# Performance work log

Hardware: AMD Instinct MI355X
Metric: run time of the kernel (lower is better)

The kernel has to match this reference:

```python
import jax, jax.numpy as jnp
import numpy as np
import math

MODEL_DIM = 2048
NUM_EXPERTS = 64
N_TOKENS = 16384
CAPACITY_FACTOR = 1.0
MIN_CAPACITY = 8
THRESHOLD = 0.5


def _threshold_gating(logits):
    # Faithful jax translation of main_thresholdGating (training path, threshold>0).
    # Note: the torch code truncates sorted columns to the data-dependent
    # explore_top_k_num; we keep the full E columns instead. This is exactly
    # equivalent: dropped columns are all-unchosen (importance 0), and using
    # arange(E,0,-1) instead of arange(K,0,-1) shifts every chosen importance
    # by the same constant (E-K), which preserves the per-expert top-k order.
    N, E = logits.shape
    capacity = max(int(math.ceil(N / E * CAPACITY_FACTOR)), MIN_CAPACITY)  # static

    gates = jax.nn.softmax(logits, axis=1)                    # [N,E]
    indices1 = jnp.argmax(gates, axis=1)                      # top-1 expert per token
    mask1 = jax.nn.one_hot(indices1, E, dtype=gates.dtype)    # [N,E]

    # sorted gates + cumsum threshold selection
    gates_sorted, gates_idx = jax.lax.top_k(gates, E)         # [N,E] descending
    cum = jnp.cumsum(gates_sorted, axis=-1)
    chosen = (cum - gates_sorted) < THRESHOLD                 # [N,E] bool
    chosen = chosen.at[:, 0].set(True)                        # always keep top-1

    # scatter importance = rank-priority + gate prob into expert columns
    rank_imp = jnp.arange(E, 0, -1, dtype=gates.dtype)[None, :] + gates_sorted
    imp = jnp.where(chosen, rank_imp, jnp.zeros_like(rank_imp))
    row = jnp.arange(N)[:, None]
    # gates_idx rows are permutations of experts -> no scatter collisions
    tam = jnp.zeros((N, E), gates.dtype).at[row, gates_idx].set(imp)  # [N,E]

    # capacity truncation: per expert column keep the `capacity` tokens with
    # highest importance
    top_idx = jax.lax.top_k(tam.T, capacity)[1]               # [E, capacity]
    keep = jnp.zeros((N, E), gates.dtype).at[top_idx, jnp.arange(E)[:, None]].set(1.0)
    final_mask = ((tam * keep) > 0).astype(gates.dtype)       # [N,E]

    combine_weights = gates * final_mask

    # load-balancing aux loss (GShard style)
    me = jnp.mean(gates, axis=0)
    ce = jnp.mean(mask1, axis=0)
    l_aux = jnp.sum(me * ce) * E
    return l_aux, combine_weights


def setup_inputs() -> dict:
    key = jax.random.key(0)
    kx, kw = jax.random.split(key)
    x = jax.random.normal(kx, (N_TOKENS, MODEL_DIM), dtype=jnp.float32)
    # gate weight of wg = Linear(model_dim, num_experts, bias=False)
    W = jax.random.normal(kw, (NUM_EXPERTS, MODEL_DIM), dtype=jnp.float32) / math.sqrt(MODEL_DIM)
    return {"x": x, "W": W}


def reference(x, W):
    logits = x @ W.T                                          # [N,E]
    l_aux, combine_weights = _threshold_gating(logits)
    return l_aux, combine_weights
```

## Files before the change

kernel.cpp:

```cpp
#include <hip/hip_runtime.h>
#include <cstdint>
#include <cstddef>

#define N_TOK  16384
#define NEXP   64
#define KDIM   2048
#define CAP    256
#define NE_TOT ((size_t)N_TOK * NEXP)

typedef __attribute__((ext_vector_type(8))) short short8;
typedef __attribute__((ext_vector_type(4))) float f32x4;

__device__ __forceinline__ unsigned short bf16_rtn(float f) {
  unsigned u = __float_as_uint(f);
  u += 0x7FFFu + ((u >> 16) & 1u);
  return (unsigned short)(u >> 16);
}
__device__ __forceinline__ float bf16_f(unsigned short h) {
  return __uint_as_float((unsigned)h << 16);
}
__device__ __forceinline__ f32x4 MF(short8 a, short8 b, f32x4 c) {
  return __builtin_amdgcn_mfma_f32_16x16x32_bf16(a, b, c, 0, 0, 0);
}

__global__ __launch_bounds__(256) void wdigits(const float* __restrict__ W,
    unsigned short* __restrict__ Wh, unsigned short* __restrict__ Wl,
    unsigned short* __restrict__ Wq) {
  const int e = (int)blockIdx.x * 256 + (int)threadIdx.x;
  const int col = e >> 11;
  const int k   = e & 2047;
  const float w = W[(size_t)col * KDIM + k];
  const unsigned short h = bf16_rtn(w);
  const float r1 = w - bf16_f(h);
  const unsigned short lo = bf16_rtn(r1);
  const float r2 = r1 - bf16_f(lo);
  const unsigned short q = bf16_rtn(r2);
  const size_t idx = (size_t)(k >> 3) * 512 + (size_t)col * 8 + (k & 7);
  Wh[idx] = h; Wl[idx] = lo; Wq[idx] = q;
}

__device__ __forceinline__ void cvt8(float4 a, float4 b,
                                     short8& h, short8& lo, short8& q) {
  float f[8] = {a.x, a.y, a.z, a.w, b.x, b.y, b.z, b.w};
#pragma unroll
  for (int j = 0; j < 8; ++j) {
    unsigned short hh = bf16_rtn(f[j]);
    float r1 = f[j] - bf16_f(hh);
    unsigned short ll = bf16_rtn(r1);
    float r2 = r1 - bf16_f(ll);
    h[j] = (short)hh; lo[j] = (short)ll; q[j] = (short)bf16_rtn(r2);
  }
}

template <int KS>
__global__ __launch_bounds__(256) void gemm_mfma(const float* __restrict__ x,
    const unsigned short* __restrict__ Wh, const unsigned short* __restrict__ Wl,
    const unsigned short* __restrict__ Wq, float* __restrict__ part) {
  constexpr int NSTEP = (KDIM / KS) / 32;
  const int tid = (int)threadIdx.x;
  const int l   = tid & 63;
  const int wv  = tid >> 6;
  const int gw  = (int)blockIdx.x * 4 + wv;
  const int mt  = gw / KS;
  const int ks  = gw % KS;
  const int row0 = mt * 32;
  const int kBeg = ks * (KDIM / KS);
  const int lr = l & 15;
  const int lk = l >> 4;

  f32x4 acc00 = {0.f,0.f,0.f,0.f}, acc01 = {0.f,0.f,0.f,0.f};
  f32x4 acc02 = {0.f,0.f,0.f,0.f}, acc03 = {0.f,0.f,0.f,0.f};
  f32x4 acc10 = {0.f,0.f,0.f,0.f}, acc11 = {0.f,0.f,0.f,0.f};
  f32x4 acc12 = {0.f,0.f,0.f,0.f}, acc13 = {0.f,0.f,0.f,0.f};

  const float* pa0 = x + (size_t)(row0 + lr) * KDIM + kBeg + lk * 8;
  const float* pa1 = pa0 + (size_t)16 * KDIM;
  const size_t bbase = ((size_t)((kBeg >> 3) + lk)) * 64 + lr;
  const short8* BH = (const short8*)Wh + bbase;
  const short8* BL = (const short8*)Wl + bbase;
  const short8* BQ = (const short8*)Wq + bbase;

  float4 A0a = *(const float4*)pa0;
  float4 A0b = *(const float4*)(pa0 + 4);
  float4 A1a = *(const float4*)pa1;
  float4 A1b = *(const float4*)(pa1 + 4);

  for (int s = 0; s < NSTEP; ++s) {
    const int so = s * 256;
    short8 b_h0 = BH[so +  0], b_h1 = BH[so + 16], b_h2 = BH[so + 32], b_h3 = BH[so + 48];
    short8 b_l0 = BL[so +  0], b_l1 = BL[so + 16], b_l2 = BL[so + 32], b_l3 = BL[so + 48];
    short8 b_q0 = BQ[so +  0], b_q1 = BQ[so + 16], b_q2 = BQ[so + 32], b_q3 = BQ[so + 48];
    float4 N0a = A0a, N0b = A0b, N1a = A1a, N1b = A1b;
    if (s + 1 < NSTEP) {
      pa0 += 32; pa1 += 32;
      N0a = *(const float4*)pa0;
      N0b = *(const float4*)(pa0 + 4);
      N1a = *(const float4*)pa1;
      N1b = *(const float4*)(pa1 + 4);
    }
    short8 a_h0, a_l0, a_q0, a_h1, a_l1, a_q1;
    cvt8(A0a, A0b, a_h0, a_l0, a_q0);
    cvt8(A1a, A1b, a_h1, a_l1, a_q1);

#define CT_BLOCK(ACC0, ACC1, BH_, BL_, BQ_)                          \
    ACC0 = MF(a_h0, BH_, ACC0); ACC0 = MF(a_h0, BL_, ACC0);          \
    ACC0 = MF(a_l0, BH_, ACC0); ACC0 = MF(a_l0, BL_, ACC0);          \
    ACC0 = MF(a_q0, BH_, ACC0); ACC0 = MF(a_h0, BQ_, ACC0);          \
    ACC1 = MF(a_h1, BH_, ACC1); ACC1 = MF(a_h1, BL_, ACC1);          \
    ACC1 = MF(a_l1, BH_, ACC1); ACC1 = MF(a_l1, BL_, ACC1);          \
    ACC1 = MF(a_q1, BH_, ACC1); ACC1 = MF(a_h1, BQ_, ACC1);

    CT_BLOCK(acc00, acc10, b_h0, b_l0, b_q0)
    CT_BLOCK(acc01, acc11, b_h1, b_l1, b_q1)
    CT_BLOCK(acc02, acc12, b_h2, b_l2, b_q2)
    CT_BLOCK(acc03, acc13, b_h3, b_l3, b_q3)
#undef CT_BLOCK

    A0a = N0a; A0b = N0b; A1a = N1a; A1b = N1b;
  }

  float* pout = part + (size_t)ks * NE_TOT;
  const int rb = row0 + lk * 4;
#pragma unroll
  for (int r = 0; r < 4; ++r) {
    pout[(size_t)(rb + r) * 64 +  0 + lr] = acc00[r];
    pout[(size_t)(rb + r) * 64 + 16 + lr] = acc01[r];
    pout[(size_t)(rb + r) * 64 + 32 + lr] = acc02[r];
    pout[(size_t)(rb + r) * 64 + 48 + lr] = acc03[r];
    pout[(size_t)(rb + 16 + r) * 64 +  0 + lr] = acc10[r];
    pout[(size_t)(rb + 16 + r) * 64 + 16 + lr] = acc11[r];
    pout[(size_t)(rb + 16 + r) * 64 + 32 + lr] = acc12[r];
    pout[(size_t)(rb + 16 + r) * 64 + 48 + lr] = acc13[r];
  }
}

template <int KS>
__global__ __launch_bounds__(1024) void gate_rows(const float* __restrict__ part,
                                                  float* __restrict__ gatesT,
                                                  float* __restrict__ tamT) {
  __shared__ float gt[64][65];
  __shared__ float tt[64][65];
  const int tid  = (int)threadIdx.x;
  const int lane = tid & 63;
  const int wid  = tid >> 6;
  const int row0 = (int)blockIdx.x * 64;

#pragma unroll
  for (int r = 0; r < 4; ++r) {
    const int rloc = wid * 4 + r;
    const size_t base = (size_t)(row0 + rloc) * NEXP;

    float logit = 0.f;
#pragma unroll
    for (int s = 0; s < KS; ++s)
      logit += part[(size_t)s * NE_TOT + base + lane];

    float m = logit;
#pragma unroll
    for (int off = 32; off > 0; off >>= 1) m = fmaxf(m, __shfl_xor(m, off));
    float p = expf(logit - m);
    float sum = p;
#pragma unroll
    for (int off = 32; off > 0; off >>= 1) sum += __shfl_xor(sum, off);
    const float gate = p / sum;

    float g = gate;
    int idx = lane;
#pragma unroll
    for (int k = 2; k <= 64; k <<= 1) {
#pragma unroll
      for (int j = k >> 1; j > 0; j >>= 1) {
        float og = __shfl_xor(g, j);
        int   oi = __shfl_xor(idx, j);
        bool iLower     = (lane & j) == 0;
        bool wantFirst  = ((lane & k) == 0) ? iLower : !iLower;
        bool otherFirst = (og > g) || (og == g && oi < idx);
        if (otherFirst == wantFirst) { g = og; idx = oi; }
      }
    }

    float cum = g;
#pragma unroll
    for (int off = 1; off < 64; off <<= 1) {
      float t = __shfl_up(cum, off);
      if (lane >= off) cum += t;
    }
    const bool chosen = (lane == 0) || ((cum - g) < 0.5f);
    const float imp = chosen ? ((float)(NEXP - lane) + g) : 0.f;

    gt[rloc][lane] = gate;
    tt[rloc][idx]  = imp;
  }
  __syncthreads();

#pragma unroll
  for (int p = 0; p < 4; ++p) {
    const int e = p * 16 + wid;
    gatesT[(size_t)e * N_TOK + row0 + lane] = gt[lane][e];
    tamT  [(size_t)e * N_TOK + row0 + lane] = tt[lane][e];
  }
}

__global__ __launch_bounds__(1024) void expert_select(
    const float* __restrict__ gatesT, const float* __restrict__ tamT,
    float* __restrict__ me_sum, int* __restrict__ ce_cnt,
    float* __restrict__ combT) {
  __shared__ int   hist16[16][256];
  __shared__ int   hist[256];
  __shared__ float wsum[16];
  __shared__ int   wice[16];
  __shared__ int   wnnz[16];
  __shared__ int   wcnt[16];
  __shared__ unsigned sh_prefix;
  __shared__ int      sh_k;
  __shared__ int      sh_nnz;

  const int e    = (int)blockIdx.x;
  const int tid  = (int)threadIdx.x;
  const int lane = tid & 63;
  const int wid  = tid >> 6;
  const float* tcol = tamT   + (size_t)e * N_TOK;
  const float* gcol = gatesT + (size_t)e * N_TOK;

  float gsum = 0.f;
  int ccnt = 0, nnzl = 0;
#pragma unroll
  for (int k = 0; k < 4; ++k) {
    int i4 = tid + k * 1024;
    float4 tv = reinterpret_cast<const float4*>(tcol)[i4];
    float4 gv = reinterpret_cast<const float4*>(gcol)[i4];
    gsum += gv.x + gv.y + gv.z + gv.w;
    ccnt += (tv.x > 64.f) + (tv.y > 64.f) + (tv.z > 64.f) + (tv.w > 64.f);
    nnzl += (tv.x != 0.f) + (tv.y != 0.f) + (tv.z != 0.f) + (tv.w != 0.f);
  }
#pragma unroll
  for (int off = 32; off > 0; off >>= 1) {
    gsum += __shfl_xor(gsum, off);
    ccnt += __shfl_xor(ccnt, off);
    nnzl += __shfl_xor(nnzl, off);
  }
  if (lane == 0) { wsum[wid] = gsum; wice[wid] = ccnt; wnnz[wid] = nnzl; }
  __syncthreads();
  if (tid == 0) {
    float t = 0.f; int c = 0, nz = 0;
    for (int w = 0; w < 16; ++w) { t += wsum[w]; c += wice[w]; nz += wnnz[w]; }
    me_sum[e] = t; ce_cnt[e] = c; sh_nnz = nz;
  }
  __syncthreads();
  const int nnz = sh_nnz;

  unsigned vstar = 0u;
  int meq = 0;
  if (nnz > CAP) {
    unsigned prefix = 0;
    int krem = CAP;
    for (int round = 0; round < 4; ++round) {
      const int shift = 24 - 8 * round;
      const unsigned maskAbove =
          (round == 0) ? 0u : (0xFFFFFFFFu << (shift + 8));
      for (int z = tid; z < 16 * 256; z += 1024) ((int*)hist16)[z] = 0;
      __syncthreads();
#pragma unroll
      for (int k = 0; k < 16; ++k) {
        unsigned u = __float_as_uint(tcol[tid + k * 1024]);
        if (u != 0u && (u & maskAbove) == prefix)
          atomicAdd(&hist16[wid][(u >> shift) & 255], 1);
      }
      __syncthreads();
      if (tid < 256) {
        int s = 0;
#pragma unroll
        for (int w = 0; w < 16; ++w) s += hist16[w][tid];
        hist[tid] = s;
      }
      __syncthreads();
      if (wid == 0) {
        int h0 = hist[lane * 4 + 0], h1 = hist[lane * 4 + 1];
        int h2 = hist[lane * 4 + 2], h3 = hist[lane * 4 + 3];
        int lsum = h0 + h1 + h2 + h3;
        int suf = lsum;
#pragma unroll
        for (int off = 1; off < 64; off <<= 1) {
          int t = __shfl_down(suf, off);
          if (lane + off < 64) suf += t;
        }
        int above = suf - lsum;
        int S3 = above + h3, S2 = S3 + h2, S1 = S2 + h1, S0 = S1 + h0;
        if (S0 >= krem && S1    < krem) { sh_prefix = prefix | ((unsigned)(lane*4+0) << shift); sh_k = krem - S1;    }
        if (S1 >= krem && S2    < krem) { sh_prefix = prefix | ((unsigned)(lane*4+1) << shift); sh_k = krem - S2;    }
        if (S2 >= krem && S3    < krem) { sh_prefix = prefix | ((unsigned)(lane*4+2) << shift); sh_k = krem - S3;    }
        if (S3 >= krem && above < krem) { sh_prefix = prefix | ((unsigned)(lane*4+3) << shift); sh_k = krem - above; }
      }
      __syncthreads();
      prefix = sh_prefix;
      krem   = sh_k;
      __syncthreads();
    }
    vstar = prefix;
    meq   = krem;
  }

  float4 tq[4];
#pragma unroll
  for (int q = 0; q < 4; ++q)
    tq[q] = reinterpret_cast<const float4*>(tcol)[tid * 4 + q];
  int cnt = 0;
#pragma unroll
  for (int q = 0; q < 4; ++q) {
    cnt += (__float_as_uint(tq[q].x) == vstar);
    cnt += (__float_as_uint(tq[q].y) == vstar);
    cnt += (__float_as_uint(tq[q].z) == vstar);
    cnt += (__float_as_uint(tq[q].w) == vstar);
  }
  int inc = cnt;
#pragma unroll
  for (int off = 1; off < 64; off <<= 1) {
    int t = __shfl_up(inc, off);
    if (lane >= off) inc += t;
  }
  if (lane == 63) wcnt[wid] = inc;
  __syncthreads();
  if (tid == 0) {
    int run = 0;
    for (int w = 0; w < 16; ++w) { int t = wcnt[w]; wcnt[w] = run; run += t; }
  }
  __syncthreads();
  int exc = (inc - cnt) + wcnt[wid];

  float* ccol = combT + (size_t)e * N_TOK;
#pragma unroll
  for (int q = 0; q < 4; ++q) {
    float4 gq = reinterpret_cast<const float4*>(gcol)[tid * 4 + q];
    float ov[4];
    const float tv[4] = {tq[q].x, tq[q].y, tq[q].z, tq[q].w};
    const float gv[4] = {gq.x, gq.y, gq.z, gq.w};
#pragma unroll
    for (int j = 0; j < 4; ++j) {
      unsigned u = __float_as_uint(tv[j]);
      bool keep;
      if (u == vstar) { keep = (exc < meq); ++exc; }
      else            { keep = (u > vstar); }
      ov[j] = (keep && u != 0u) ? gv[j] : 0.f;
    }
    reinterpret_cast<float4*>(ccol)[tid * 4 + q] =
        make_float4(ov[0], ov[1], ov[2], ov[3]);
  }
}

__global__ __launch_bounds__(1024) void transpose_out(
    const float* __restrict__ combT, float* __restrict__ out1) {
  __shared__ float tile[64][65];
  const int tid  = (int)threadIdx.x;
  const int lane = tid & 63;
  const int wid  = tid >> 6;
  const int tok0 = (int)blockIdx.x * 64;
#pragma unroll
  for (int p = 0; p < 4; ++p) {
    const int e = p * 16 + wid;
    tile[lane][e] = combT[(size_t)e * N_TOK + tok0 + lane];
  }
  __syncthreads();
#pragma unroll
  for (int q = 0; q < 4; ++q) {
    const int tok = q * 16 + wid;
    out1[(size_t)(tok0 + tok) * NEXP + lane] = tile[tok][lane];
  }
}

__global__ void aux_loss(const float* __restrict__ me_sum,
                         const int* __restrict__ ce_cnt,
                         float* __restrict__ out0) {
  const int lane = (int)threadIdx.x;
  float v = (me_sum[lane] / (float)N_TOK) *
            ((float)ce_cnt[lane] / (float)N_TOK);
#pragma unroll
  for (int off = 32; off > 0; off >>= 1) v += __shfl_xor(v, off);
  if (lane == 0) out0[0] = v * (float)NEXP;
}

extern "C" void kernel_launch(void* const* d_in, const int* in_sizes, int n_in,
                              void* d_out, int out_size, void* d_ws, size_t ws_size,
                              hipStream_t stream) {
  const float* x = (const float*)d_in[0];
  const float* W = (const float*)d_in[1];
  float* out = (float*)d_out;
  float* ws  = (float*)d_ws;

  const bool ks8 = ws_size >= (size_t)(8 + 2) * NE_TOT * 4 + 1024;
  const int  KS  = ks8 ? 8 : 4;

  float* part   = ws;
  float* combT  = ws;
  float* gatesT = ws + (size_t)KS * NE_TOT;
  float* tamT   = gatesT + NE_TOT;
  float* me     = tamT + NE_TOT;
  int*   ce     = (int*)(me + 64);

  unsigned short* Wh = (unsigned short*)gatesT;
  unsigned short* Wl = Wh + (size_t)NEXP * KDIM;
  unsigned short* Wq = Wl + (size_t)NEXP * KDIM;

  wdigits<<<(NEXP * KDIM) / 256, 256, 0, stream>>>(W, Wh, Wl, Wq);
  if (ks8) gemm_mfma<8><<<128 * 8, 256, 0, stream>>>(x, Wh, Wl, Wq, part);
  else     gemm_mfma<4><<<128 * 4, 256, 0, stream>>>(x, Wh, Wl, Wq, part);
  if (ks8) gate_rows<8><<<N_TOK / 64, 1024, 0, stream>>>(part, gatesT, tamT);
  else     gate_rows<4><<<N_TOK / 64, 1024, 0, stream>>>(part, gatesT, tamT);
  expert_select<<<NEXP, 1024, 0, stream>>>(gatesT, tamT, me, ce, combT);
  transpose_out<<<N_TOK / 64, 1024, 0, stream>>>(combT, out + 1);
  aux_loss<<<1, 64, 0, stream>>>(me, ce, out);
}
```

Before: 82.06 us.

## Software-pipeline B loads in GEMM, remap blocks by k-split, fold aux loss into transpose

The GEMM inner loop now loads each B column group just before it is needed and prefetches the next one while the current MFMA block runs. This cuts the number of live B registers, and launch_bounds(256,4) is added to aim for higher occupancy. Blocks are remapped so that each block takes one k-split and four consecutive m-tiles, which changes how x and W are reused in cache. The separate aux_loss kernel is folded into transpose_out to save one launch. The register cap may cause spills, and the later B loads may expose more latency.

Result: no change. 81.67 us (-0.5%).

```diff
diff --git a/kernel.cpp b/kernel.cpp
--- a/kernel.cpp
+++ b/kernel.cpp
@@ -53,16 +53,15 @@
 }
 
 template <int KS>
-__global__ __launch_bounds__(256) void gemm_mfma(const float* __restrict__ x,
+__global__ __launch_bounds__(256, 4) void gemm_mfma(const float* __restrict__ x,
     const unsigned short* __restrict__ Wh, const unsigned short* __restrict__ Wl,
     const unsigned short* __restrict__ Wq, float* __restrict__ part) {
   constexpr int NSTEP = (KDIM / KS) / 32;
   const int tid = (int)threadIdx.x;
   const int l   = tid & 63;
   const int wv  = tid >> 6;
-  const int gw  = (int)blockIdx.x * 4 + wv;
-  const int mt  = gw / KS;
-  const int ks  = gw % KS;
+  const int ks  = (int)blockIdx.x >> 7;
+  const int mt  = (((int)blockIdx.x & 127) << 2) + wv;
   const int row0 = mt * 32;
   const int kBeg = ks * (KDIM / KS);
   const int lr = l & 15;
@@ -84,39 +83,43 @@
   float4 A0b = *(const float4*)(pa0 + 4);
   float4 A1a = *(const float4*)pa1;
   float4 A1b = *(const float4*)(pa1 + 4);
+  short8 bh = BH[0], bl = BL[0], bq = BQ[0];
 
   for (int s = 0; s < NSTEP; ++s) {
     const int so = s * 256;
-    short8 b_h0 = BH[so +  0], b_h1 = BH[so + 16], b_h2 = BH[so + 32], b_h3 = BH[so + 48];
-    short8 b_l0 = BL[so +  0], b_l1 = BL[so + 16], b_l2 = BL[so + 32], b_l3 = BL[so + 48];
-    short8 b_q0 = BQ[so +  0], b_q1 = BQ[so + 16], b_q2 = BQ[so + 32], b_q3 = BQ[so + 48];
-    float4 N0a = A0a, N0b = A0b, N1a = A1a, N1b = A1b;
-    if (s + 1 < NSTEP) {
-      pa0 += 32; pa1 += 32;
-      N0a = *(const float4*)pa0;
-      N0b = *(const float4*)(pa0 + 4);
-      N1a = *(const float4*)pa1;
-      N1b = *(const float4*)(pa1 + 4);
-    }
     short8 a_h0, a_l0, a_q0, a_h1, a_l1, a_q1;
     cvt8(A0a, A0b, a_h0, a_l0, a_q0);
     cvt8(A1a, A1b, a_h1, a_l1, a_q1);
-
-#define CT_BLOCK(ACC0, ACC1, BH_, BL_, BQ_)                          \
-    ACC0 = MF(a_h0, BH_, ACC0); ACC0 = MF(a_h0, BL_, ACC0);          \
-    ACC0 = MF(a_l0, BH_, ACC0); ACC0 = MF(a_l0, BL_, ACC0);          \
-    ACC0 = MF(a_q0, BH_, ACC0); ACC0 = MF(a_h0, BQ_, ACC0);          \
-    ACC1 = MF(a_h1, BH_, ACC1); ACC1 = MF(a_h1, BL_, ACC1);          \
-    ACC1 = MF(a_l1, BH_, ACC1); ACC1 = MF(a_l1, BL_, ACC1);          \
-    ACC1 = MF(a_q1, BH_, ACC1); ACC1 = MF(a_h1, BQ_, ACC1);
-
-    CT_BLOCK(acc00, acc10, b_h0, b_l0, b_q0)
-    CT_BLOCK(acc01, acc11, b_h1, b_l1, b_q1)
-    CT_BLOCK(acc02, acc12, b_h2, b_l2, b_q2)
-    CT_BLOCK(acc03, acc13, b_h3, b_l3, b_q3)
+    if (s + 1 < NSTEP) {
+      pa0 += 32; pa1 += 32;
+      A0a = *(const float4*)pa0;
+      A0b = *(const float4*)(pa0 + 4);
+      A1a = *(const float4*)pa1;
+      A1b = *(const float4*)(pa1 + 4);
+    }
+
+#define CT_BLOCK(ACC0, ACC1)                                         \
+    ACC0 = MF(a_h0, bh, ACC0); ACC0 = MF(a_h0, bl, ACC0);            \
+    ACC0 = MF(a_l0, bh, ACC0); ACC0 = MF(a_l0, bl, ACC0);            \
+    ACC0 = MF(a_q0, bh, ACC0); ACC0 = MF(a_h0, bq, ACC0);            \
+    ACC1 = MF(a_h1, bh, ACC1); ACC1 = MF(a_h1, bl, ACC1);            \
+    ACC1 = MF(a_l1, bh, ACC1); ACC1 = MF(a_l1, bl, ACC1);            \
+    ACC1 = MF(a_q1, bh, ACC1); ACC1 = MF(a_h1, bq, ACC1);
+
+    short8 nh = BH[so + 16], nl = BL[so + 16], nq = BQ[so + 16];
+    CT_BLOCK(acc00, acc10)
+    bh = nh; bl = nl; bq = nq;
+    nh = BH[so + 32]; nl = BL[so + 32]; nq = BQ[so + 32];
+    CT_BLOCK(acc01, acc11)
+    bh = nh; bl = nl; bq = nq;
+    nh = BH[so + 48]; nl = BL[so + 48]; nq = BQ[so + 48];
+    CT_BLOCK(acc02, acc12)
+    bh = nh; bl = nl; bq = nq;
+    const int ni = (s + 1 < NSTEP) ? so + 256 : so;
+    nh = BH[ni]; nl = BL[ni]; nq = BQ[ni];
+    CT_BLOCK(acc03, acc13)
+    bh = nh; bl = nl; bq = nq;
 #undef CT_BLOCK
-
-    A0a = N0a; A0b = N0b; A1a = N1a; A1b = N1b;
   }
 
   float* pout = part + (size_t)ks * NE_TOT;
@@ -348,7 +351,9 @@
 }
 
 __global__ __launch_bounds__(1024) void transpose_out(
-    const float* __restrict__ combT, float* __restrict__ out1) {
+    const float* __restrict__ combT, float* __restrict__ out1,
+    const float* __restrict__ me_sum, const int* __restrict__ ce_cnt,
+    float* __restrict__ out0) {
   __shared__ float tile[64][65];
   const int tid  = (int)threadIdx.x;
   const int lane = tid & 63;
@@ -365,17 +370,13 @@
     const int tok = q * 16 + wid;
     out1[(size_t)(tok0 + tok) * NEXP + lane] = tile[tok][lane];
   }
-}
-
-__global__ void aux_loss(const float* __restrict__ me_sum,
-                         const int* __restrict__ ce_cnt,
-                         float* __restrict__ out0) {
-  const int lane = (int)threadIdx.x;
-  float v = (me_sum[lane] / (float)N_TOK) *
-            ((float)ce_cnt[lane] / (float)N_TOK);
-#pragma unroll
-  for (int off = 32; off > 0; off >>= 1) v += __shfl_xor(v, off);
-  if (lane == 0) out0[0] = v * (float)NEXP;
+  if (blockIdx.x == 0 && wid == 0) {
+    float v = (me_sum[lane] / (float)N_TOK) *
+              ((float)ce_cnt[lane] / (float)N_TOK);
+#pragma unroll
+    for (int off = 32; off > 0; off >>= 1) v += __shfl_xor(v, off);
+    if (lane == 0) out0[0] = v * (float)NEXP;
+  }
 }
 
 extern "C" void kernel_launch(void* const* d_in, const int* in_sizes, int n_in,
@@ -406,6 +407,5 @@
   if (ks8) gate_rows<8><<<N_TOK / 64, 1024, 0, stream>>>(part, gatesT, tamT);
   else     gate_rows<4><<<N_TOK / 64, 1024, 0, stream>>>(part, gatesT, tamT);
   expert_select<<<NEXP, 1024, 0, stream>>>(gatesT, tamT, me, ce, combT);
-  transpose_out<<<N_TOK / 64, 1024, 0, stream>>>(combT, out + 1);
-  aux_loss<<<1, 64, 0, stream>>>(me, ce, out);
-}
+  transpose_out<<<N_TOK / 64, 1024, 0, stream>>>(combT, out + 1, me, ce, out);
+}
```
